# Optimization experiments

Measured on AMD Instinct MI355X. Metric: run time of the kernel, lower is better.

Reference implementation:

```python
import jax, jax.numpy as jnp
import numpy as np

NUM_GROUPS = 32
EPS = 1e-5


def group_norm(x, scale, bias):
    # x: [b, c, h, w]
    b, c, h, w = x.shape
    xg = x.reshape(b, NUM_GROUPS, c // NUM_GROUPS, h, w)
    mean = jnp.mean(xg, axis=(2, 3, 4), keepdims=True)
    var = jnp.var(xg, axis=(2, 3, 4), keepdims=True)
    xg = (xg - mean) * jax.lax.rsqrt(var + EPS)
    xn = xg.reshape(b, c, h, w)
    return xn * scale[None, :, None, None] + bias[None, :, None, None]


def conv1x1(x, w, b):
    # x: [b, c_in, h, w], w: [c_out, c_in], b: [c_out]
    return jnp.einsum('bchw,dc->bdhw', x, w) + b[None, :, None, None]


def setup_inputs() -> dict:
    key = jax.random.key(0)
    ks = jax.random.split(key, 11)
    B, C, H, W = 16, 512, 32, 32
    s = 1.0 / np.sqrt(C)
    inp = {
        'x': jax.random.normal(ks[0], (B, C, H, W), jnp.float32),
        'gn_scale': jnp.ones((C,), jnp.float32),
        'gn_bias': jnp.zeros((C,), jnp.float32),
        'wq': jax.random.normal(ks[1], (C, C), jnp.float32) * s,
        'bq': jnp.zeros((C,), jnp.float32),
        'wk': jax.random.normal(ks[2], (C, C), jnp.float32) * s,
        'bk': jnp.zeros((C,), jnp.float32),
        'wv': jax.random.normal(ks[3], (C, C), jnp.float32) * s,
        'bv': jnp.zeros((C,), jnp.float32),
        'wp': jax.random.normal(ks[4], (C, C), jnp.float32) * s,
        'bp': jnp.zeros((C,), jnp.float32),
    }
    return inp


def reference(x, gn_scale, gn_bias, wq, bq, wk, bk, wv, bv, wp, bp):
    b, c, h, w = x.shape
    xn = group_norm(x, gn_scale, gn_bias)
    q = conv1x1(xn, wq, bq).reshape(b, c, h * w)  # [b, c, n]
    k = conv1x1(xn, wk, bk).reshape(b, c, h * w)
    v = conv1x1(xn, wv, bv).reshape(b, c, h * w)
    # attn[b, i, j] = sum_c q[b, c, i] * k[b, c, j]
    attn = jnp.einsum('bci,bcj->bij', q, k) * (c ** -0.5)
    A = jax.nn.softmax(attn, axis=-1)
    # out[b, c, i] = sum_j A[b, i, j] * v[b, c, j]
    out = jnp.einsum('bij,bcj->bci', A, v).reshape(b, c, h, w)
    scores = conv1x1(out, wp, bp)
    return x + scores
```

## Files before the change

### kernel.cpp

```cpp
#include <hip/hip_runtime.h>

typedef __bf16 bf16x8 __attribute__((ext_vector_type(8)));
typedef float  f32x4  __attribute__((ext_vector_type(4)));

__device__ __forceinline__ unsigned short f2bf(float f) {
    union { float f; unsigned int u; } x; x.f = f;
    unsigned int r = (x.u + 0x7FFFu + ((x.u >> 16) & 1u)) >> 16;
    return (unsigned short)r;
}
__device__ __forceinline__ float bf2f(unsigned int hi) {
    union { unsigned int u; float f; } x; x.u = hi; return x.f;
}

typedef const __attribute__((address_space(1))) unsigned short gu16;
typedef __attribute__((address_space(3)))       unsigned short lu16;
__device__ __forceinline__ void gl_lds16(const unsigned short* g, unsigned short* l) {
    __builtin_amdgcn_global_load_lds((gu16*)g, (lu16*)l, 16, 0, 0);
}

__device__ __forceinline__ void stage_tiles(
    const unsigned short* __restrict__ Ab, int lda,
    const unsigned short* __restrict__ Bb, int ldb,
    int k0, unsigned short* Ad, unsigned short* Bd,
    int wave, int r0, int c0)
{
    gl_lds16(Ab + (long)r0 * lda + c0 + k0,        Ad + wave * 512);
    gl_lds16(Ab + (long)(r0 + 64) * lda + c0 + k0, Ad + 2048 + wave * 512);
    gl_lds16(Bb + (long)r0 * ldb + c0 + k0,        Bd + wave * 512);
    gl_lds16(Bb + (long)(r0 + 64) * ldb + c0 + k0, Bd + 2048 + wave * 512);
}

__device__ __forceinline__ void gemm_core_db(
    const unsigned short* __restrict__ Ab, int lda,
    const unsigned short* __restrict__ Bb, int ldb,
    int K, f32x4 (&acc)[4][4],
    unsigned short* As, unsigned short* Bs)
{
    const int tid  = threadIdx.x;
    const int lane = tid & 63;
    const int wave = tid >> 6;
    const int wm   = (wave >> 1) * 64;
    const int wn   = (wave & 1) * 64;
    const int l16  = lane & 15;
    const int quad = lane >> 4;

    const int r0 = wave * 16 + (lane >> 2);
    const int c0 = (lane & 3) * 8;

    stage_tiles(Ab, lda, Bb, ldb, 0, As, Bs, wave, r0, c0);

    int sel = 0;
    for (int k0 = 0; k0 < K; k0 += 32) {
        __syncthreads();
        if (k0 + 32 < K)
            stage_tiles(Ab, lda, Bb, ldb, k0 + 32,
                        As + (sel ^ 1) * 4096, Bs + (sel ^ 1) * 4096, wave, r0, c0);

        const unsigned short* Ap = As + sel * 4096;
        const unsigned short* Bp = Bs + sel * 4096;
        bf16x8 af[4], bfr[4];
        #pragma unroll
        for (int mi = 0; mi < 4; mi++)
            af[mi] = *(const bf16x8*)&Ap[(wm + mi * 16 + l16) * 32 + quad * 8];
        #pragma unroll
        for (int ni = 0; ni < 4; ni++)
            bfr[ni] = *(const bf16x8*)&Bp[(wn + ni * 16 + l16) * 32 + quad * 8];
        #pragma unroll
        for (int mi = 0; mi < 4; mi++)
            #pragma unroll
            for (int ni = 0; ni < 4; ni++)
                acc[mi][ni] = __builtin_amdgcn_mfma_f32_16x16x32_bf16(af[mi], bfr[ni], acc[mi][ni], 0, 0, 0);
        sel ^= 1;
    }
}

template<typename OutT, bool TRANS_OUT, bool HAS_BIAS, bool HAS_RESID,
         bool EXP_SUM, bool ROW_SCALE>
__global__ __launch_bounds__(256) void gemm_k(
    const unsigned short* __restrict__ Ag, long sA, int lda,
    const unsigned short* __restrict__ Bg, long sB, int ldb,
    OutT* __restrict__ Cg, long sC, int ldc,
    const float* __restrict__ bias,
    const float* __restrict__ resid, long sR,
    float* __restrict__ lsum, long sL,
    float alpha, int K)
{
    __shared__ __align__(16) unsigned short As[2 * 4096];
    __shared__ __align__(16) unsigned short Bs[2 * 4096];

    const unsigned short* Ab = Ag + (long)blockIdx.z * sA + (long)(blockIdx.y * 128) * lda;
    const unsigned short* Bb = Bg + (long)blockIdx.z * sB + (long)(blockIdx.x * 128) * ldb;

    f32x4 acc[4][4] = {};
    gemm_core_db(Ab, lda, Bb, ldb, K, acc, As, Bs);

    const int lane = threadIdx.x & 63;
    const int wave = threadIdx.x >> 6;
    const int l16  = lane & 15;
    const int quad = lane >> 4;
    const int mb = blockIdx.y * 128 + (wave >> 1) * 64;
    const int nb = blockIdx.x * 128 + (wave & 1) * 64;

    #pragma unroll
    for (int mi = 0; mi < 4; mi++) {
        float rsum[4];
        if constexpr (EXP_SUM) { rsum[0] = rsum[1] = rsum[2] = rsum[3] = 0.f; }
        #pragma unroll
        for (int ni = 0; ni < 4; ni++) {
            f32x4 v = acc[mi][ni];
            const int m0 = mb + mi * 16 + quad * 4;
            const int n  = nb + ni * 16 + l16;
            float o[4];
            float invl;
            if constexpr (ROW_SCALE) invl = 1.f / lsum[(long)blockIdx.z * sL + n];
            #pragma unroll
            for (int r = 0; r < 4; r++) {
                float val = v[r] * alpha;
                if (HAS_BIAS) val += bias[m0 + r];
                if constexpr (EXP_SUM) { val = __expf(val); rsum[r] += val; }
                if constexpr (ROW_SCALE) val *= invl;
                o[r] = val;
            }
            if constexpr (!TRANS_OUT) {
                const long base = (long)blockIdx.z * sC;
                #pragma unroll
                for (int r = 0; r < 4; r++) {
                    float val = o[r];
                    if (HAS_RESID) val += resid[(long)blockIdx.z * sR + (long)(m0 + r) * ldc + n];
                    long idx = base + (long)(m0 + r) * ldc + n;
                    if constexpr (sizeof(OutT) == 2) ((unsigned short*)Cg)[idx] = f2bf(val);
                    else                              ((float*)Cg)[idx] = val;
                }
            } else {
                const long idx = (long)blockIdx.z * sC + (long)n * ldc + m0;
                if constexpr (sizeof(OutT) == 2) {
                    ushort4 p; p.x = f2bf(o[0]); p.y = f2bf(o[1]); p.z = f2bf(o[2]); p.w = f2bf(o[3]);
                    *(ushort4*)((unsigned short*)Cg + idx) = p;
                } else {
                    float4 p; p.x = o[0]; p.y = o[1]; p.z = o[2]; p.w = o[3];
                    *(float4*)((float*)Cg + idx) = p;
                }
            }
        }
        if constexpr (EXP_SUM) {
            const int m0 = mb + mi * 16 + quad * 4;
            #pragma unroll
            for (int r = 0; r < 4; r++) {
                float s = rsum[r];
                s += __shfl_xor(s, 1); s += __shfl_xor(s, 2);
                s += __shfl_xor(s, 4); s += __shfl_xor(s, 8);
                if (l16 == 0)
                    atomicAdd(&lsum[(long)blockIdx.z * sL + m0 + r], s);
            }
        }
    }
}

__global__ __launch_bounds__(256) void qkv_k(
    const unsigned short* __restrict__ Wqkv,
    const unsigned short* __restrict__ xnT,
    unsigned short* __restrict__ qT,
    unsigned short* __restrict__ kT,
    unsigned short* __restrict__ vB,
    const float* __restrict__ bqkv)
{
    __shared__ __align__(16) unsigned short As[2 * 4096];
    __shared__ __align__(16) unsigned short Bs[2 * 4096];

    const unsigned short* Ab = Wqkv + (long)(blockIdx.y * 128) * 512;
    const unsigned short* Bb = xnT + (long)blockIdx.z * 524288 + (long)(blockIdx.x * 128) * 512;

    f32x4 acc[4][4] = {};
    gemm_core_db(Ab, 512, Bb, 512, 512, acc, As, Bs);

    const int lane = threadIdx.x & 63;
    const int wave = threadIdx.x >> 6;
    const int l16  = lane & 15;
    const int quad = lane >> 4;
    const int mb = blockIdx.y * 128 + (wave >> 1) * 64;
    const int nb = blockIdx.x * 128 + (wave & 1) * 64;

    const int mat = blockIdx.y >> 2;
    const long zb = (long)blockIdx.z * 524288;

    #pragma unroll
    for (int mi = 0; mi < 4; mi++) {
        #pragma unroll
        for (int ni = 0; ni < 4; ni++) {
            f32x4 v = acc[mi][ni];
            const int m0 = mb + mi * 16 + quad * 4;
            const int n  = nb + ni * 16 + l16;
            float o[4];
            #pragma unroll
            for (int r = 0; r < 4; r++) o[r] = v[r] + bqkv[m0 + r];
            const int ml = m0 & 511;
            if (mat == 2) {
                #pragma unroll
                for (int r = 0; r < 4; r++)
                    vB[zb + (long)(ml + r) * 1024 + n] = f2bf(o[r]);
            } else {
                unsigned short* dst = (mat == 0) ? qT : kT;
                ushort4 p; p.x = f2bf(o[0]); p.y = f2bf(o[1]); p.z = f2bf(o[2]); p.w = f2bf(o[3]);
                *(ushort4*)(dst + zb + (long)n * 512 + ml) = p;
            }
        }
    }
}

__global__ __launch_bounds__(256) void gn_k(
    const float* __restrict__ x, const float* __restrict__ gsc,
    const float* __restrict__ gbi, unsigned short* __restrict__ xnT)
{
    __shared__ __align__(16) unsigned short ln[16 * 1024];
    __shared__ float red[8];
    const int b = blockIdx.y, g = blockIdx.x;
    const int tid = threadIdx.x, lane = tid & 63, wv = tid >> 6;

    const float4* x4 = (const float4*)(x + ((long)b * 512 + g * 16) * 1024);
    float4 vals[16];
    float s = 0.f, ss = 0.f;
    #pragma unroll
    for (int i = 0; i < 16; i++) {
        float4 v = x4[tid + i * 256];
        vals[i] = v;
        s  += v.x + v.y + v.z + v.w;
        ss += v.x * v.x + v.y * v.y + v.z * v.z + v.w * v.w;
    }
    for (int o = 32; o; o >>= 1) { s += __shfl_down(s, o); ss += __shfl_down(ss, o); }
    if (lane == 0) { red[wv * 2] = s; red[wv * 2 + 1] = ss; }
    __syncthreads();
    const float S  = red[0] + red[2] + red[4] + red[6];
    const float SS = red[1] + red[3] + red[5] + red[7];
    const float mean = S * (1.f / 16384.f);
    const float var  = SS * (1.f / 16384.f) - mean * mean;
    const float inv  = rsqrtf(var + 1e-5f);

    #pragma unroll
    for (int i = 0; i < 16; i++) {
        const int idx = tid + i * 256;
        const int c   = idx >> 8;
        const float sc = gsc[g * 16 + c] * inv;
        const float bi = gbi[g * 16 + c] - mean * sc;
        float4 v = vals[i];
        ushort4 p;
        p.x = f2bf(v.x * sc + bi); p.y = f2bf(v.y * sc + bi);
        p.z = f2bf(v.z * sc + bi); p.w = f2bf(v.w * sc + bi);
        ((ushort4*)ln)[idx] = p;
    }
    __syncthreads();

    unsigned short* op = xnT + (long)b * 1024 * 512 + g * 16;
    for (int rep = 0; rep < 4; rep++) {
        const int n = rep * 256 + tid;
        union { unsigned short u[16]; uint4 v[2]; } t;
        #pragma unroll
        for (int c = 0; c < 16; c++) t.u[c] = ln[c * 1024 + n];
        *(uint4*)&op[(long)n * 512]     = t.v[0];
        *(uint4*)&op[(long)n * 512 + 8] = t.v[1];
    }
}

__global__ __launch_bounds__(256) void wconv_k(
    const float* __restrict__ w0, const float* __restrict__ w1,
    const float* __restrict__ w2, const float* __restrict__ w3,
    const float* __restrict__ b0, const float* __restrict__ b1,
    const float* __restrict__ b2,
    unsigned short* __restrict__ out, float* __restrict__ bqkv,
    float* __restrict__ lsum)
{
    const int m = blockIdx.y;
    const int i = blockIdx.x * 256 + threadIdx.x;
    if (m == 4) {
        if (i < 384) {
            const int which = i >> 7, off = i & 127;
            const float* src = (which == 0) ? b0 : (which == 1) ? b1 : b2;
            ((float4*)bqkv)[i] = ((const float4*)src)[off];
        }
        if (i < 16384) lsum[i] = 0.f;
        return;
    }
    const float* src = (m == 0) ? w0 : (m == 1) ? w1 : (m == 2) ? w2 : w3;
    float4 v = ((const float4*)src)[i];
    ushort4 o; o.x = f2bf(v.x); o.y = f2bf(v.y); o.z = f2bf(v.z); o.w = f2bf(v.w);
    ((ushort4*)(out + (long)m * 262144))[i] = o;
}

extern "C" void kernel_launch(void* const* d_in, const int* in_sizes, int n_in,
                              void* d_out, int out_size, void* d_ws, size_t ws_size,
                              hipStream_t stream)
{
    const float* x   = (const float*)d_in[0];
    const float* gsc = (const float*)d_in[1];
    const float* gbi = (const float*)d_in[2];
    const float* wq  = (const float*)d_in[3];
    const float* bq  = (const float*)d_in[4];
    const float* wk  = (const float*)d_in[5];
    const float* bk  = (const float*)d_in[6];
    const float* wv  = (const float*)d_in[7];
    const float* bv  = (const float*)d_in[8];
    const float* wp  = (const float*)d_in[9];
    const float* bp  = (const float*)d_in[10];
    float* out = (float*)d_out;

    char* ws = (char*)d_ws;
    unsigned short* xnT = (unsigned short*)(ws);
    unsigned short* qT  = (unsigned short*)(ws + 16777216);
    unsigned short* kT  = (unsigned short*)(ws + 33554432);
    unsigned short* vB  = (unsigned short*)(ws + 50331648);
    unsigned short* Sb  = (unsigned short*)(ws + 67108864);
    unsigned short* Wb  = (unsigned short*)(ws + 100663296);
    float*          bqkv= (float*)        (ws + 102760448);
    float*          Lb  = (float*)        (ws + 102768640);
    unsigned short* OT  = xnT;

    const long sBCN = 512L * 1024;

    wconv_k<<<dim3(256, 5), 256, 0, stream>>>(wq, wk, wv, wp, bq, bk, bv, Wb, bqkv, Lb);
    gn_k<<<dim3(32, 16), 256, 0, stream>>>(x, gsc, gbi, xnT);

    qkv_k<<<dim3(8, 12, 16), 256, 0, stream>>>(Wb, xnT, qT, kT, vB, bqkv);

    gemm_k<unsigned short, false, false, false, true, false>
        <<<dim3(8, 8, 16), 256, 0, stream>>>(
        qT, sBCN, 512, kT, sBCN, 512, Sb, 1048576L, 1024, nullptr, nullptr, 0,
        Lb, 1024, 0.044194173824159216f, 512);

    gemm_k<unsigned short, true, false, false, false, true>
        <<<dim3(8, 4, 16), 256, 0, stream>>>(
        vB, sBCN, 1024, Sb, 1048576L, 1024, OT, sBCN, 512,
        nullptr, nullptr, 0, Lb, 1024, 1.f, 1024);

    gemm_k<float, false, true, true, false, false>
        <<<dim3(8, 4, 16), 256, 0, stream>>>(
        Wb + 786432, 0, 512, OT, sBCN, 512, out, sBCN, 1024, bp, x, sBCN,
        nullptr, 0, 1.f, 512);
}
```

Measured before the change: 238.9 us.

## Fuse QK^T, softmax and PV into a single attention kernel

```diff
diff --git a/kernel.cpp b/kernel.cpp
--- a/kernel.cpp
+++ b/kernel.cpp
@@ -7,9 +7,6 @@
     union { float f; unsigned int u; } x; x.f = f;
     unsigned int r = (x.u + 0x7FFFu + ((x.u >> 16) & 1u)) >> 16;
     return (unsigned short)r;
-}
-__device__ __forceinline__ float bf2f(unsigned int hi) {
-    union { unsigned int u; float f; } x; x.u = hi; return x.f;
 }
 
 typedef const __attribute__((address_space(1))) unsigned short gu16;
@@ -74,15 +71,13 @@
     }
 }
 
-template<typename OutT, bool TRANS_OUT, bool HAS_BIAS, bool HAS_RESID,
-         bool EXP_SUM, bool ROW_SCALE>
+template<typename OutT, bool TRANS_OUT, bool HAS_BIAS, bool HAS_RESID>
 __global__ __launch_bounds__(256) void gemm_k(
     const unsigned short* __restrict__ Ag, long sA, int lda,
     const unsigned short* __restrict__ Bg, long sB, int ldb,
     OutT* __restrict__ Cg, long sC, int ldc,
     const float* __restrict__ bias,
     const float* __restrict__ resid, long sR,
-    float* __restrict__ lsum, long sL,
     float alpha, int K)
 {
     __shared__ __align__(16) unsigned short As[2 * 4096];
@@ -103,22 +98,16 @@
 
     #pragma unroll
     for (int mi = 0; mi < 4; mi++) {
-        float rsum[4];
-        if constexpr (EXP_SUM) { rsum[0] = rsum[1] = rsum[2] = rsum[3] = 0.f; }
         #pragma unroll
         for (int ni = 0; ni < 4; ni++) {
             f32x4 v = acc[mi][ni];
             const int m0 = mb + mi * 16 + quad * 4;
             const int n  = nb + ni * 16 + l16;
             float o[4];
-            float invl;
-            if constexpr (ROW_SCALE) invl = 1.f / lsum[(long)blockIdx.z * sL + n];
             #pragma unroll
             for (int r = 0; r < 4; r++) {
                 float val = v[r] * alpha;
                 if (HAS_BIAS) val += bias[m0 + r];
-                if constexpr (EXP_SUM) { val = __expf(val); rsum[r] += val; }
-                if constexpr (ROW_SCALE) val *= invl;
                 o[r] = val;
             }
             if constexpr (!TRANS_OUT) {
@@ -142,17 +131,6 @@
                 }
             }
         }
-        if constexpr (EXP_SUM) {
-            const int m0 = mb + mi * 16 + quad * 4;
-            #pragma unroll
-            for (int r = 0; r < 4; r++) {
-                float s = rsum[r];
-                s += __shfl_xor(s, 1); s += __shfl_xor(s, 2);
-                s += __shfl_xor(s, 4); s += __shfl_xor(s, 8);
-                if (l16 == 0)
-                    atomicAdd(&lsum[(long)blockIdx.z * sL + m0 + r], s);
-            }
-        }
     }
 }
 
@@ -205,6 +183,144 @@
             }
         }
     }
+}
+
+__global__ __launch_bounds__(256, 2) void attn_k(
+    const unsigned short* __restrict__ qT,
+    const unsigned short* __restrict__ kT,
+    const unsigned short* __restrict__ vB,
+    unsigned short* __restrict__ OT)
+{
+    __shared__ __align__(16) unsigned short Qs[16 * 1024];
+    __shared__ __align__(16) unsigned short Ks[2 * 4096];
+    __shared__ __align__(16) unsigned short Ps[32 * 136];
+    __shared__ float redS[4][32];
+
+    const int b   = blockIdx.y;
+    const int i0  = blockIdx.x * 32;
+    const int tid = threadIdx.x;
+    const int w    = tid >> 6;
+    const int lane = tid & 63;
+    const int l16  = lane & 15;
+    const int quad = lane >> 4;
+    const long zb  = (long)b * 524288;
+
+    {
+        const uint4* qg = (const uint4*)(qT + zb + (long)i0 * 512);
+        #pragma unroll
+        for (int it = 0; it < 8; it++) {
+            const int f = it * 256 + tid;
+            const int i = f >> 6;
+            const int c = (f & 63) * 8;
+            uint4 v = qg[f];
+            *(uint4*)&Qs[(c >> 5) * 1024 + i * 32 + (c & 31)] = v;
+        }
+    }
+
+    const int krow = w * 16 + (lane >> 2);
+    const int kcol = (lane & 3) * 8;
+    const float scale = 0.044194173824159216f;
+
+    f32x4 oacc[8][2] = {};
+    float psum[2] = {0.f, 0.f};
+
+    __syncthreads();
+
+    for (int jt = 0; jt < 8; jt++) {
+        const int j0 = jt * 128;
+
+        bf16x8 vreg[4][8];
+        #pragma unroll
+        for (int kb = 0; kb < 4; kb++)
+            #pragma unroll
+            for (int mt = 0; mt < 8; mt++)
+                vreg[kb][mt] = *(const bf16x8*)(vB + zb +
+                    (long)(w * 128 + mt * 16 + l16) * 1024 + j0 + kb * 32 + quad * 8);
+
+        f32x4 sacc[2][2] = {};
+        for (int r8 = 0; r8 < 8; r8++) {
+            __syncthreads();
+            #pragma unroll
+            for (int sub = 0; sub < 2; sub++)
+                #pragma unroll
+                for (int ch = 0; ch < 2; ch++)
+                    gl_lds16(kT + zb + (long)(j0 + ch * 64 + krow) * 512 + r8 * 64 + sub * 32 + kcol,
+                             Ks + sub * 4096 + ch * 2048 + w * 512);
+            __syncthreads();
+
+            #pragma unroll
+            for (int sub = 0; sub < 2; sub++) {
+                bf16x8 kf[2], qf[2];
+                #pragma unroll
+                for (int mt = 0; mt < 2; mt++)
+                    kf[mt] = *(const bf16x8*)&Ks[sub * 4096 + (w * 32 + mt * 16 + l16) * 32 + quad * 8];
+                const int panel = r8 * 2 + sub;
+                #pragma unroll
+                for (int nt = 0; nt < 2; nt++)
+                    qf[nt] = *(const bf16x8*)&Qs[panel * 1024 + (nt * 16 + l16) * 32 + quad * 8];
+                #pragma unroll
+                for (int mt = 0; mt < 2; mt++)
+                    #pragma unroll
+                    for (int nt = 0; nt < 2; nt++)
+                        sacc[mt][nt] = __builtin_amdgcn_mfma_f32_16x16x32_bf16(kf[mt], qf[nt], sacc[mt][nt], 0, 0, 0);
+            }
+        }
+
+        #pragma unroll
+        for (int mt = 0; mt < 2; mt++)
+            #pragma unroll
+            for (int nt = 0; nt < 2; nt++) {
+                f32x4 v = sacc[mt][nt];
+                float e0 = __expf(v[0] * scale), e1 = __expf(v[1] * scale);
+                float e2 = __expf(v[2] * scale), e3 = __expf(v[3] * scale);
+                psum[nt] += (e0 + e1) + (e2 + e3);
+                ushort4 p; p.x = f2bf(e0); p.y = f2bf(e1); p.z = f2bf(e2); p.w = f2bf(e3);
+                *(ushort4*)&Ps[(nt * 16 + l16) * 136 + w * 32 + mt * 16 + quad * 4] = p;
+            }
+        __syncthreads();
+
+        #pragma unroll
+        for (int kb = 0; kb < 4; kb++) {
+            bf16x8 pf[2];
+            #pragma unroll
+            for (int nt = 0; nt < 2; nt++)
+                pf[nt] = *(const bf16x8*)&Ps[(nt * 16 + l16) * 136 + kb * 32 + quad * 8];
+            #pragma unroll
+            for (int mt = 0; mt < 8; mt++)
+                #pragma unroll
+                for (int nt = 0; nt < 2; nt++)
+                    oacc[mt][nt] = __builtin_amdgcn_mfma_f32_16x16x32_bf16(vreg[kb][mt], pf[nt], oacc[mt][nt], 0, 0, 0);
+        }
+    }
+
+    #pragma unroll
+    for (int nt = 0; nt < 2; nt++) {
+        psum[nt] += __shfl_xor(psum[nt], 16);
+        psum[nt] += __shfl_xor(psum[nt], 32);
+    }
+    __syncthreads();
+    if (quad == 0) { redS[w][l16] = psum[0]; redS[w][16 + l16] = psum[1]; }
+    __syncthreads();
+
+    float invl[2];
+    #pragma unroll
+    for (int nt = 0; nt < 2; nt++) {
+        const int ii = nt * 16 + l16;
+        invl[nt] = 1.f / ((redS[0][ii] + redS[1][ii]) + (redS[2][ii] + redS[3][ii]));
+    }
+
+    #pragma unroll
+    for (int mt = 0; mt < 8; mt++)
+        #pragma unroll
+        for (int nt = 0; nt < 2; nt++) {
+            f32x4 v = oacc[mt][nt];
+            const int i = i0 + nt * 16 + l16;
+            const int c = w * 128 + mt * 16 + quad * 4;
+            ushort4 p;
+            p.x = f2bf(v[0] * invl[nt]); p.y = f2bf(v[1] * invl[nt]);
+            p.z = f2bf(v[2] * invl[nt]); p.w = f2bf(v[3] * invl[nt]);
+            *(ushort4*)(OT + zb + (long)i * 512 + c) = p;
+        }
 }
 
 __global__ __launch_bounds__(256) void gn_k(
@@ -265,8 +381,7 @@
     const float* __restrict__ w2, const float* __restrict__ w3,
     const float* __restrict__ b0, const float* __restrict__ b1,
     const float* __restrict__ b2,
-    unsigned short* __restrict__ out, float* __restrict__ bqkv,
-    float* __restrict__ lsum)
+    unsigned short* __restrict__ out, float* __restrict__ bqkv)
 {
     const int m = blockIdx.y;
     const int i = blockIdx.x * 256 + threadIdx.x;
@@ -276,7 +391,6 @@
             const float* src = (which == 0) ? b0 : (which == 1) ? b1 : b2;
             ((float4*)bqkv)[i] = ((const float4*)src)[off];
         }
-        if (i < 16384) lsum[i] = 0.f;
         return;
     }
     const float* src = (m == 0) ? w0 : (m == 1) ? w1 : (m == 2) ? w2 : w3;
@@ -307,31 +421,19 @@
     unsigned short* qT  = (unsigned short*)(ws + 16777216);
     unsigned short* kT  = (unsigned short*)(ws + 33554432);
     unsigned short* vB  = (unsigned short*)(ws + 50331648);
-    unsigned short* Sb  = (unsigned short*)(ws + 67108864);
     unsigned short* Wb  = (unsigned short*)(ws + 100663296);
     float*          bqkv= (float*)        (ws + 102760448);
-    float*          Lb  = (float*)        (ws + 102768640);
     unsigned short* OT  = xnT;
 
     const long sBCN = 512L * 1024;
 
-    wconv_k<<<dim3(256, 5), 256, 0, stream>>>(wq, wk, wv, wp, bq, bk, bv, Wb, bqkv, Lb);
+    wconv_k<<<dim3(256, 5), 256, 0, stream>>>(wq, wk, wv, wp, bq, bk, bv, Wb, bqkv);
     gn_k<<<dim3(32, 16), 256, 0, stream>>>(x, gsc, gbi, xnT);
 
     qkv_k<<<dim3(8, 12, 16), 256, 0, stream>>>(Wb, xnT, qT, kT, vB, bqkv);
 
-    gemm_k<unsigned short, false, false, false, true, false>
-        <<<dim3(8, 8, 16), 256, 0, stream>>>(
-        qT, sBCN, 512, kT, sBCN, 512, Sb, 1048576L, 1024, nullptr, nullptr, 0,
-        Lb, 1024, 0.044194173824159216f, 512);
-
-    gemm_k<unsigned short, true, false, false, false, true>
-        <<<dim3(8, 4, 16), 256, 0, stream>>>(
-        vB, sBCN, 1024, Sb, 1048576L, 1024, OT, sBCN, 512,
-        nullptr, nullptr, 0, Lb, 1024, 1.f, 1024);
-
-    gemm_k<float, false, true, true, false, false>
-        <<<dim3(8, 4, 16), 256, 0, stream>>>(
-        Wb + 786432, 0, 512, OT, sBCN, 512, out, sBCN, 1024, bp, x, sBCN,
-        nullptr, 0, 1.f, 512);
-}
+    attn_k<<<dim3(32, 16), 256, 0, stream>>>(qT, kT, vB, OT);
+
+    gemm_k<float, false, true, true><<<dim3(8, 4, 16), 256, 0, stream>>>(
+        Wb + 786432, 0, 512, OT, sBCN, 512, out, sBCN, 1024, bp, x, sBCN, 1.f, 512);
+}
```

Result: slower. 282.7 us (+18.3%).
